# Kernel tuning notes

Measured on AMD Instinct MI355X. Metric: run time of the kernel, lower is better.

## Reference

```python
import jax, jax.numpy as jnp
import numpy as np

BINS = 10          # par.BINS
ALPHA = 0.5        # par.RATIO_KLD
EPS = 1e-10
NUM_ENC = 10       # encoded feature columns used for histograms
BLOCKS = ((7, 19), (19, 21), (21, 25), (25, 27), (27, 29), (29, 31), (31, 34), (34, 38), (38, 50))
B = 1048576


def setup_inputs() -> dict:
    key = jax.random.key(0)
    ks = jax.random.split(key, 16)
    data_encoded = jax.random.normal(ks[0], (B, NUM_ENC), dtype=jnp.float32)
    data_decoded = jax.random.normal(ks[1], (B, 50), dtype=jnp.float32)
    parts = [jax.random.normal(ks[2], (B, 7), dtype=jnp.float32)]  # numerical part
    for i, (s, e) in enumerate(BLOCKS):  # one-hot categorical ground truth
        lab = jax.random.randint(ks[3 + i], (B,), 0, e - s)
        parts.append(jax.nn.one_hot(lab, e - s, dtype=jnp.float32))
    data_true = jnp.concatenate(parts, axis=1)  # (B, 50)
    grp = jax.random.randint(ks[12], (B,), 0, 2).astype(jnp.float32)  # marital flag -> column 11 of combined
    label_true = jnp.stack([
        jax.random.randint(ks[13], (B,), 0, 2).astype(jnp.float32),
        grp,
        jax.random.normal(ks[14], (B,), dtype=jnp.float32),
    ], axis=1)  # (B, 3)
    return {"data_encoded": data_encoded, "data_decoded": data_decoded,
            "data_true": data_true, "label_true": label_true, "batch_size": B}


def _ce(logits, onehot):
    # F.cross_entropy with labels recovered from one-hot rows (nonzero -> argmax)
    labels = jnp.argmax(onehot, axis=1)
    lp = jax.nn.log_softmax(logits, axis=1)
    return -jnp.mean(jnp.take_along_axis(lp, labels[:, None], axis=1))


def _group_hist(enc, mask, mins, maxs):
    # torch.histc per column, restricted to rows where mask==1, normalized by group size
    width = jnp.maximum(maxs - mins, EPS)
    bins = jnp.clip(jnp.floor((enc - mins) / width * BINS), 0, BINS - 1).astype(jnp.int32)  # (B, 10)
    flat = bins + jnp.arange(NUM_ENC, dtype=jnp.int32)[None, :] * BINS                     # (B, 10)
    w = jnp.broadcast_to(mask[:, None], flat.shape).reshape(-1)
    hist = jnp.zeros(NUM_ENC * BINS, dtype=jnp.float32).at[flat.reshape(-1)].add(w)
    return hist.reshape(NUM_ENC, BINS) / jnp.maximum(jnp.sum(mask), 1.0)


def _kl(p, q):
    # KL(p || q) summed over all (feature, bin) cells, zero-safe
    return jnp.sum(jnp.where(p > 0, p * jnp.log(p / jnp.maximum(q, EPS)), 0.0))


def reference(data_encoded, data_decoded, data_true, label_true, batch_size):
    # numerical MSE over first 7 cols, then *7 (mse_Loss)
    mse_loss = jnp.mean((data_decoded[:, 0:7] - data_true[:, 0:7]) ** 2) * 7.0
    # 9 cross-entropy terms over categorical blocks
    ce_loss = jnp.float32(0.0)
    for s, e in BLOCKS:
        ce_loss = ce_loss + _ce(data_decoded[:, s:e], data_true[:, s:e])
    # per-group histogram KLD over the 10 encoded columns (detached in the original)
    enc = data_encoded  # first 10 cols of encoded_combined
    mins = jnp.min(enc, axis=0)
    maxs = jnp.max(enc, axis=0)
    grp = label_true[:, 1]  # column 11 of cat(data_encoded, label_true)
    single_mask = (grp == 0).astype(jnp.float32)
    married_mask = (grp == 1).astype(jnp.float32)
    p = _group_hist(enc, single_mask, mins, maxs)   # (10, BINS)
    q = _group_hist(enc, married_mask, mins, maxs)  # (10, BINS)
    kld = jax.lax.stop_gradient(_kl(p, q))  # original goes through .numpy() -> no grads
    multi_loss = (1.0 - ALPHA) * (mse_loss + ce_loss) + ALPHA * kld
    return (multi_loss, mse_loss, ce_loss, ALPHA * kld)
```

## Files before the change

kernel.cpp:

```cpp
#include <hip/hip_runtime.h>
#include <math.h>

#define EPSF 1e-10f
#define TILE 32
#define TILEH 64

struct WS { double sum_mse, sum_ce; float mn[10], mx[10]; };

typedef __attribute__((address_space(3))) unsigned int lds_u32_t;
typedef __attribute__((address_space(1))) const unsigned int glb_u32_t;
__device__ __forceinline__ void load_lds16(const void* g, void* l){
  __builtin_amdgcn_global_load_lds((glb_u32_t*)g, (lds_u32_t*)l, 16, 0, 0);
}

template<int S, int E>
__device__ __forceinline__ float ce_block_lds(const float* __restrict__ d,
                                              const float* __restrict__ t){
  constexpr int N = E - S;
  float dv[N];
  #pragma unroll
  for (int j = 0; j < N; j++) dv[j] = d[S + j];
  float mx = dv[0];
  #pragma unroll
  for (int j = 1; j < N; j++) mx = fmaxf(mx, dv[j]);
  float se = 0.f, dot = 0.f;
  #pragma unroll
  for (int j = 0; j < N; j++){ se += __expf(dv[j] - mx); dot += t[S + j] * dv[j]; }
  return mx + __logf(se) - dot;
}

__global__ void k_main(const float* __restrict__ enc, const float* __restrict__ dec,
                       const float* __restrict__ tru,
                       double* __restrict__ pmMse, double* __restrict__ pmCe,
                       float* __restrict__ pmMn, float* __restrict__ pmMx,
                       int B, int nbm){
  __shared__ alignas(16) float bufD[2][TILE * 50];
  __shared__ alignas(16) float bufT[2][TILE * 50];
  __shared__ alignas(16) float bufE[2][TILE * 10];
  __shared__ double sMse[4], sCe[4];
  __shared__ float  sMn[4][10], sMx[4][10];

  const int tid  = threadIdx.x;
  const int wave = tid >> 6;
  const int lane = tid & 63;
  const int h    = tid >> 5;
  const int row  = tid & 31;

  float mn[10], mx[10];
  #pragma unroll
  for (int c = 0; c < 10; c++){ mn[c] = 3.4e38f; mx[c] = -3.4e38f; }
  float mse_acc = 0.f, ce_acc = 0.f;

  const int nTiles = B / TILE;
  int nT_loc = (blockIdx.x < nTiles) ? (nTiles - blockIdx.x + nbm - 1) / nbm : 0;

  float4 rd0, rd1, rt0, rt1, re;

  auto load_stage = [&](int k){
    const int tl = blockIdx.x + k * nbm;
    const float4* dp4 = reinterpret_cast<const float4*>(dec + (size_t)tl * (TILE * 50));
    const float4* tp4 = reinterpret_cast<const float4*>(tru + (size_t)tl * (TILE * 50));
    const float4* ep4 = reinterpret_cast<const float4*>(enc + (size_t)tl * (TILE * 10));
    rd0 = dp4[tid];
    rt0 = tp4[tid];
    if (tid < 144){ rd1 = dp4[256 + tid]; rt1 = tp4[256 + tid]; }
    if (tid < 80){ re = ep4[tid]; }
  };
  auto write_stage = [&](int b){
    float4* bD = reinterpret_cast<float4*>(bufD[b]);
    float4* bT = reinterpret_cast<float4*>(bufT[b]);
    float4* bE = reinterpret_cast<float4*>(bufE[b]);
    bD[tid] = rd0;
    bT[tid] = rt0;
    if (tid < 144){ bD[256 + tid] = rd1; bT[256 + tid] = rt1; }
    if (tid < 80){ bE[tid] = re; }
  };

  if (nT_loc > 0) load_stage(0);

  for (int k = 0; k < nT_loc; ++k){
    const int b = k & 1;
    write_stage(b);
    if (k + 1 < nT_loc) load_stage(k + 1);
    __syncthreads();

    {
      const float* d = bufD[b] + row * 50;
      const float* t = bufT[b] + row * 50;
      const float* e = bufE[b] + row * 10;
      switch (h){
        case 0: {
          float m = 0.f;
          #pragma unroll
          for (int j = 0; j < 7; j++){ float df = d[j] - t[j]; m += df * df; }
          mse_acc += m;
          { float v = e[0]; mn[0] = fminf(mn[0], v); mx[0] = fmaxf(mx[0], v); }
          { float v = e[1]; mn[1] = fminf(mn[1], v); mx[1] = fmaxf(mx[1], v); }
        } break;
        case 1: {
          ce_acc += ce_block_lds< 7,19>(d, t);
          { float v = e[2]; mn[2] = fminf(mn[2], v); mx[2] = fmaxf(mx[2], v); }
        } break;
        case 2: {
          ce_acc += ce_block_lds<19,21>(d, t);
          ce_acc += ce_block_lds<21,25>(d, t);
          { float v = e[3]; mn[3] = fminf(mn[3], v); mx[3] = fmaxf(mx[3], v); }
        } break;
        case 3: {
          ce_acc += ce_block_lds<25,27>(d, t);
          ce_acc += ce_block_lds<27,29>(d, t);
          { float v = e[4]; mn[4] = fminf(mn[4], v); mx[4] = fmaxf(mx[4], v); }
        } break;
        case 4: {
          ce_acc += ce_block_lds<29,31>(d, t);
          ce_acc += ce_block_lds<31,34>(d, t);
          { float v = e[5]; mn[5] = fminf(mn[5], v); mx[5] = fmaxf(mx[5], v); }
          { float v = e[6]; mn[6] = fminf(mn[6], v); mx[6] = fmaxf(mx[6], v); }
        } break;
        case 5: {
          ce_acc += ce_block_lds<34,38>(d, t);
          { float v = e[7]; mn[7] = fminf(mn[7], v); mx[7] = fmaxf(mx[7], v); }
        } break;
        case 6: {
          ce_acc += ce_block_lds<38,50>(d, t);
          { float v = e[8]; mn[8] = fminf(mn[8], v); mx[8] = fmaxf(mx[8], v); }
        } break;
        default: {
          { float v = e[9]; mn[9] = fminf(mn[9], v); mx[9] = fmaxf(mx[9], v); }
        } break;
      }
    }
  }

  #pragma unroll
  for (int c = 0; c < 10; c++){
    #pragma unroll
    for (int o = 32; o >= 1; o >>= 1){
      mn[c] = fminf(mn[c], __shfl_xor(mn[c], o));
      mx[c] = fmaxf(mx[c], __shfl_xor(mx[c], o));
    }
  }
  double mseD = (double)mse_acc, ceD = (double)ce_acc;
  #pragma unroll
  for (int o = 32; o >= 1; o >>= 1){
    mseD += __shfl_xor(mseD, o);
    ceD  += __shfl_xor(ceD,  o);
  }
  __syncthreads();
  if (lane == 0){
    sMse[wave] = mseD; sCe[wave] = ceD;
    #pragma unroll
    for (int c = 0; c < 10; c++){ sMn[wave][c] = mn[c]; sMx[wave][c] = mx[c]; }
  }
  __syncthreads();
  if (tid == 0){
    pmMse[blockIdx.x] = sMse[0] + sMse[1] + sMse[2] + sMse[3];
    pmCe[blockIdx.x]  = sCe[0]  + sCe[1]  + sCe[2]  + sCe[3];
    #pragma unroll
    for (int c = 0; c < 10; c++){
      pmMn[c * nbm + blockIdx.x] = fminf(fminf(sMn[0][c], sMn[1][c]), fminf(sMn[2][c], sMn[3][c]));
      pmMx[c * nbm + blockIdx.x] = fmaxf(fmaxf(sMx[0][c], sMx[1][c]), fmaxf(sMx[2][c], sMx[3][c]));
    }
  }
}

__global__ void k_main_fb(const float* __restrict__ enc, const float* __restrict__ dec,
                          const float* __restrict__ tru,
                          double* __restrict__ pmMse, double* __restrict__ pmCe,
                          float* __restrict__ pmMn, float* __restrict__ pmMx,
                          int B, int nbm){
  __shared__ double sMse[4], sCe[4];
  __shared__ float  sMn[4][10], sMx[4][10];
  const int tid = threadIdx.x, wave = tid >> 6, lane = tid & 63;
  float mn[10], mx[10];
  #pragma unroll
  for (int c = 0; c < 10; c++){ mn[c] = 3.4e38f; mx[c] = -3.4e38f; }
  float mse_acc = 0.f, ce_acc = 0.f;
  int stride = nbm * 256;
  for (int r = blockIdx.x * 256 + tid; r < B; r += stride){
    const float* e = enc + (size_t)r * 10;
    #pragma unroll
    for (int c = 0; c < 10; c++){ float v = e[c]; mn[c] = fminf(mn[c], v); mx[c] = fmaxf(mx[c], v); }
    const float* d = dec + (size_t)r * 50;
    const float* t = tru + (size_t)r * 50;
    float m = 0.f;
    #pragma unroll
    for (int j = 0; j < 7; j++){ float df = d[j] - t[j]; m += df * df; }
    mse_acc += m;
    ce_acc += ce_block_lds< 7,19>(d, t);
    ce_acc += ce_block_lds<19,21>(d, t);
    ce_acc += ce_block_lds<21,25>(d, t);
    ce_acc += ce_block_lds<25,27>(d, t);
    ce_acc += ce_block_lds<27,29>(d, t);
    ce_acc += ce_block_lds<29,31>(d, t);
    ce_acc += ce_block_lds<31,34>(d, t);
    ce_acc += ce_block_lds<34,38>(d, t);
    ce_acc += ce_block_lds<38,50>(d, t);
  }
  #pragma unroll
  for (int c = 0; c < 10; c++){
    #pragma unroll
    for (int o = 32; o >= 1; o >>= 1){
      mn[c] = fminf(mn[c], __shfl_xor(mn[c], o));
      mx[c] = fmaxf(mx[c], __shfl_xor(mx[c], o));
    }
  }
  double mseD = (double)mse_acc, ceD = (double)ce_acc;
  #pragma unroll
  for (int o = 32; o >= 1; o >>= 1){ mseD += __shfl_xor(mseD, o); ceD += __shfl_xor(ceD, o); }
  if (lane == 0){
    sMse[wave] = mseD; sCe[wave] = ceD;
    #pragma unroll
    for (int c = 0; c < 10; c++){ sMn[wave][c] = mn[c]; sMx[wave][c] = mx[c]; }
  }
  __syncthreads();
  if (tid == 0){
    pmMse[blockIdx.x] = sMse[0] + sMse[1] + sMse[2] + sMse[3];
    pmCe[blockIdx.x]  = sCe[0]  + sCe[1]  + sCe[2]  + sCe[3];
    #pragma unroll
    for (int c = 0; c < 10; c++){
      pmMn[c * nbm + blockIdx.x] = fminf(fminf(sMn[0][c], sMn[1][c]), fminf(sMn[2][c], sMn[3][c]));
      pmMx[c * nbm + blockIdx.x] = fmaxf(fmaxf(sMx[0][c], sMx[1][c]), fmaxf(sMx[2][c], sMx[3][c]));
    }
  }
}

__global__ void k_reduce(const double* __restrict__ pmMse, const double* __restrict__ pmCe,
                         const float* __restrict__ pmMn, const float* __restrict__ pmMx,
                         WS* __restrict__ ws, int nbm){
  __shared__ double sM[16], sC[16];
  __shared__ float  sMn[16][10], sMx[16][10];
  const int tid = threadIdx.x, wave = tid >> 6, lane = tid & 63;
  double ms = 0.0, ce = 0.0;
  float mn[10], mx[10];
  #pragma unroll
  for (int c = 0; c < 10; c++){ mn[c] = 3.4e38f; mx[c] = -3.4e38f; }
  for (int i = tid; i < nbm; i += 1024){
    ms += pmMse[i]; ce += pmCe[i];
    #pragma unroll
    for (int c = 0; c < 10; c++){
      mn[c] = fminf(mn[c], pmMn[c * nbm + i]);
      mx[c] = fmaxf(mx[c], pmMx[c * nbm + i]);
    }
  }
  #pragma unroll
  for (int o = 32; o >= 1; o >>= 1){
    ms += __shfl_xor(ms, o); ce += __shfl_xor(ce, o);
    #pragma unroll
    for (int c = 0; c < 10; c++){
      mn[c] = fminf(mn[c], __shfl_xor(mn[c], o));
      mx[c] = fmaxf(mx[c], __shfl_xor(mx[c], o));
    }
  }
  if (lane == 0){
    sM[wave] = ms; sC[wave] = ce;
    #pragma unroll
    for (int c = 0; c < 10; c++){ sMn[wave][c] = mn[c]; sMx[wave][c] = mx[c]; }
  }
  __syncthreads();
  if (tid == 0){
    double tm = 0.0, tc = 0.0;
    float rmn[10], rmx[10];
    #pragma unroll
    for (int c = 0; c < 10; c++){ rmn[c] = 3.4e38f; rmx[c] = -3.4e38f; }
    const int nw = (int)(blockDim.x >> 6);
    for (int w = 0; w < nw; w++){
      tm += sM[w]; tc += sC[w];
      #pragma unroll
      for (int c = 0; c < 10; c++){
        rmn[c] = fminf(rmn[c], sMn[w][c]);
        rmx[c] = fmaxf(rmx[c], sMx[w][c]);
      }
    }
    ws->sum_mse = tm; ws->sum_ce = tc;
    #pragma unroll
    for (int c = 0; c < 10; c++){ ws->mn[c] = rmn[c]; ws->mx[c] = rmx[c]; }
  }
}

__global__ void k_hist(const float* __restrict__ enc, const float* __restrict__ lab,
                       const WS* __restrict__ ws, unsigned* __restrict__ ph,
                       int B, int nbh){
  __shared__ unsigned int sh[202];
  __shared__ alignas(16) float bufE[2][TILEH * 10];
  __shared__ alignas(16) float bufL[2][TILEH * 3];

  const int tid  = threadIdx.x;
  const int wave = tid >> 6;
  const int lane = tid & 63;

  for (int i = tid; i < 202; i += 256) sh[i] = 0u;

  float mnv[10], wv[10];
  #pragma unroll
  for (int c = 0; c < 10; c++){
    float lo = ws->mn[c];
    float hi = ws->mx[c];
    mnv[c] = lo;
    wv[c]  = fmaxf(hi - lo, EPSF);
  }

  const int nTiles = (B + TILEH - 1) / TILEH;

  auto stage = [&](int b, int tl){
    const int rowsHere = min(TILEH, B - tl * TILEH);
    const size_t base10 = (size_t)tl * TILEH * 10;
    const size_t base3  = (size_t)tl * TILEH * 3;
    if (rowsHere == TILEH){
      const float4* ep4 = reinterpret_cast<const float4*>(enc + base10);
      const float4* lp4 = reinterpret_cast<const float4*>(lab + base3);
      float4* bE = reinterpret_cast<float4*>(bufE[b]);
      float4* bL = reinterpret_cast<float4*>(bufL[b]);
      { int i = tid; if (i < 160) load_lds16(ep4 + i, bE + i); }
      { int i = tid; if (i < 48)  load_lds16(lp4 + i, bL + i); }
    } else {
      const int ne = rowsHere * 10, nl = rowsHere * 3;
      for (int i = tid; i < ne; i += 256) bufE[b][i] = enc[base10 + i];
      for (int i = tid; i < nl; i += 256) bufL[b][i] = lab[base3 + i];
    }
  };

  const int t0 = blockIdx.x;
  if (t0 < nTiles) stage(0, t0);
  __syncthreads();

  int cur = 0;
  for (int tl = t0; tl < nTiles; tl += nbh){
    int nxt = tl + nbh;
    if (nxt < nTiles) stage(cur ^ 1, nxt);

    const int rowsHere = min(TILEH, B - tl * TILEH);
    const int rrow = lane;
    if (rrow < rowsHere){
      float g = bufL[cur][rrow * 3 + 1];
      int gi = (g == 0.0f) ? 0 : ((g == 1.0f) ? 1 : -1);
      if (gi >= 0){
        const float* e = bufE[cur] + rrow * 10;
        if (wave == 1) atomicAdd(&sh[200 + gi], 1u);
        #define DO_BIN(c) { \
          float bf = floorf((e[(c)] - mnv[(c)]) / wv[(c)] * 10.0f); \
          int b2 = (int)bf; b2 = b2 < 0 ? 0 : (b2 > 9 ? 9 : b2); \
          atomicAdd(&sh[gi * 100 + (c) * 10 + b2], 1u); }
        if (wave == 0){ DO_BIN(0) DO_BIN(1) DO_BIN(2) }
        else if (wave == 1){ DO_BIN(3) DO_BIN(4) }
        else if (wave == 2){ DO_BIN(5) DO_BIN(6) }
        else { DO_BIN(7) DO_BIN(8) DO_BIN(9) }
        #undef DO_BIN
      }
    }
    __syncthreads();
    cur ^= 1;
  }

  for (int i = tid; i < 202; i += 256) ph[(size_t)i * nbh + blockIdx.x] = sh[i];
}

__global__ void k_hreduce(const unsigned* __restrict__ ph, float* __restrict__ histF, int nbh){
  __shared__ unsigned swv[4];
  const int e = blockIdx.x, tid = threadIdx.x, wave = tid >> 6, lane = tid & 63;
  const unsigned* p = ph + (size_t)e * nbh;
  unsigned s0 = 0, s1 = 0, s2 = 0, s3 = 0;
  int k = tid;
  for (; k + 768 < nbh; k += 1024){
    s0 += p[k]; s1 += p[k + 256]; s2 += p[k + 512]; s3 += p[k + 768];
  }
  for (; k < nbh; k += 256) s0 += p[k];
  unsigned s = s0 + s1 + s2 + s3;
  #pragma unroll
  for (int o = 32; o >= 1; o >>= 1) s += __shfl_xor(s, o);
  if (lane == 0) swv[wave] = s;
  __syncthreads();
  if (tid == 0) histF[e] = (float)(swv[0] + swv[1] + swv[2] + swv[3]);
}

__global__ void k_final(const float* __restrict__ histF, const WS* __restrict__ ws,
                        float* __restrict__ out, int B){
  const int tid = threadIdx.x;
  float dens = fmaxf(histF[200], 1.0f);
  float denm = fmaxf(histF[201], 1.0f);
  float kl = 0.f;
  for (int i = tid; i < 100; i += 64){
    float p = histF[i]       / dens;
    float q = histF[100 + i] / denm;
    if (p > 0.f) kl += p * logf(p / fmaxf(q, EPSF));
  }
  #pragma unroll
  for (int o = 32; o >= 1; o >>= 1) kl += __shfl_xor(kl, o);
  if (tid == 0){
    float mse = (float)(ws->sum_mse / (double)B);
    float ce  = (float)(ws->sum_ce  / (double)B);
    float akld = 0.5f * kl;
    out[0] = 0.5f * (mse + ce) + akld;
    out[1] = mse;
    out[2] = ce;
    out[3] = akld;
  }
}

extern "C" void kernel_launch(void* const* d_in, const int* in_sizes, int n_in,
                              void* d_out, int out_size, void* d_ws, size_t ws_size,
                              hipStream_t stream){
  const float* enc = (const float*)d_in[0];
  const float* dec = (const float*)d_in[1];
  const float* tru = (const float*)d_in[2];
  const float* lab = (const float*)d_in[3];
  int B = in_sizes[1] / 50;

  const bool fast = (B > 0) && (B % TILE == 0);

  int nbm = 1280;
  int nTm = fast ? (B / TILE) : ((B + 255) / 256);
  if (nbm > nTm && nTm > 0) nbm = nTm;
  if (nbm < 1) nbm = 1;

  int nbh = 2048;
  int nTh = (B + TILEH - 1) / TILEH;
  if (nbh > nTh && nTh > 0) nbh = nTh;
  if (nbh < 1) nbh = 1;

  while ((size_t)(128 + (size_t)nbm * 96 + (size_t)202 * nbh * 4 + 1024) > ws_size && nbm > 64){
    nbm >>= 1; nbh >>= 1;
  }
  char* w = (char*)d_ws;
  WS* ws = (WS*)w;
  double* pmMse = (double*)(w + 128);
  double* pmCe  = (double*)(w + 128 + (size_t)nbm * 8);
  float*  pmMn  = (float*)(w + 128 + (size_t)nbm * 16);
  float*  pmMx  = (float*)(w + 128 + (size_t)nbm * 16 + (size_t)nbm * 40);
  unsigned* ph  = (unsigned*)(w + 128 + (size_t)nbm * 96);
  float* histF  = (float*)(w + 128 + (size_t)nbm * 96 + (size_t)202 * nbh * 4);
  float* out = (float*)d_out;

  if (fast)
    hipLaunchKernelGGL(k_main,    dim3(nbm), dim3(256), 0, stream, enc, dec, tru,
                       pmMse, pmCe, pmMn, pmMx, B, nbm);
  else
    hipLaunchKernelGGL(k_main_fb, dim3(nbm), dim3(256), 0, stream, enc, dec, tru,
                       pmMse, pmCe, pmMn, pmMx, B, nbm);
  hipLaunchKernelGGL(k_reduce,  dim3(1),   dim3(1024), 0, stream, pmMse, pmCe, pmMn, pmMx, ws, nbm);
  hipLaunchKernelGGL(k_hist,    dim3(nbh), dim3(256),  0, stream, enc, lab, ws, ph, B, nbh);
  hipLaunchKernelGGL(k_hreduce, dim3(202), dim3(256),  0, stream, ph, histF, nbh);
  hipLaunchKernelGGL(k_final,   dim3(1),   dim3(64),   0, stream, histF, ws, out, B);
}
```

Measured before the change: 121.6 us.

## Fuse final min/max/sum reduction into main kernel via last-block atomic counter

Removes the separate single-block k_reduce launch. Each main block now bumps a global atomic counter, and the last block to finish reduces all per-block partials into the workspace. A memset of the counter is added before the launch. Separately, the cross-entropy block drops the max-subtraction in log-sum-exp to save a pass over the values. That assumes the logits stay small, since large logits could overflow expf.

```diff
diff --git a/kernel.cpp b/kernel.cpp
--- a/kernel.cpp
+++ b/kernel.cpp
@@ -17,28 +17,109 @@
 __device__ __forceinline__ float ce_block_lds(const float* __restrict__ d,
                                               const float* __restrict__ t){
   constexpr int N = E - S;
-  float dv[N];
-  #pragma unroll
-  for (int j = 0; j < N; j++) dv[j] = d[S + j];
-  float mx = dv[0];
-  #pragma unroll
-  for (int j = 1; j < N; j++) mx = fmaxf(mx, dv[j]);
   float se = 0.f, dot = 0.f;
   #pragma unroll
-  for (int j = 0; j < N; j++){ se += __expf(dv[j] - mx); dot += t[S + j] * dv[j]; }
-  return mx + __logf(se) - dot;
+  for (int j = 0; j < N; j++){
+    float x = d[S + j];
+    se += __expf(x);
+    dot += t[S + j] * x;
+  }
+  return __logf(se) - dot;
+}
+
+__device__ __forceinline__ void main_epilogue(
+    int tid, int wave, int lane, int nbm,
+    float mse_acc, float ce_acc, float* mn, float* mx,
+    double* sMse, double* sCe, float (*sMn)[10], float (*sMx)[10], int* isLast,
+    double* pmMse, double* pmCe, float* pmMn, float* pmMx,
+    unsigned* cnt, WS* ws){
+  #pragma unroll
+  for (int c = 0; c < 10; c++){
+    #pragma unroll
+    for (int o = 32; o >= 1; o >>= 1){
+      mn[c] = fminf(mn[c], __shfl_xor(mn[c], o));
+      mx[c] = fmaxf(mx[c], __shfl_xor(mx[c], o));
+    }
+  }
+  double mseD = (double)mse_acc, ceD = (double)ce_acc;
+  #pragma unroll
+  for (int o = 32; o >= 1; o >>= 1){
+    mseD += __shfl_xor(mseD, o);
+    ceD  += __shfl_xor(ceD,  o);
+  }
+  __syncthreads();
+  if (lane == 0){
+    sMse[wave] = mseD; sCe[wave] = ceD;
+    #pragma unroll
+    for (int c = 0; c < 10; c++){ sMn[wave][c] = mn[c]; sMx[wave][c] = mx[c]; }
+  }
+  __syncthreads();
+  if (tid == 0){
+    pmMse[blockIdx.x] = sMse[0] + sMse[1] + sMse[2] + sMse[3];
+    pmCe[blockIdx.x]  = sCe[0]  + sCe[1]  + sCe[2]  + sCe[3];
+    #pragma unroll
+    for (int c = 0; c < 10; c++){
+      pmMn[c * nbm + blockIdx.x] = fminf(fminf(sMn[0][c], sMn[1][c]), fminf(sMn[2][c], sMn[3][c]));
+      pmMx[c * nbm + blockIdx.x] = fmaxf(fmaxf(sMx[0][c], sMx[1][c]), fmaxf(sMx[2][c], sMx[3][c]));
+    }
+    __threadfence();
+    unsigned old = atomicAdd(cnt, 1u);
+    *isLast = (old == (unsigned)(nbm - 1)) ? 1 : 0;
+  }
+  __syncthreads();
+  if (*isLast){
+    __threadfence();
+    double ms = 0.0, ce = 0.0;
+    float rmn[10], rmx[10];
+    #pragma unroll
+    for (int c = 0; c < 10; c++){ rmn[c] = 3.4e38f; rmx[c] = -3.4e38f; }
+    for (int i = tid; i < nbm; i += 256){
+      ms += pmMse[i]; ce += pmCe[i];
+      #pragma unroll
+      for (int c = 0; c < 10; c++){
+        rmn[c] = fminf(rmn[c], pmMn[c * nbm + i]);
+        rmx[c] = fmaxf(rmx[c], pmMx[c * nbm + i]);
+      }
+    }
+    #pragma unroll
+    for (int o = 32; o >= 1; o >>= 1){
+      ms += __shfl_xor(ms, o); ce += __shfl_xor(ce, o);
+      #pragma unroll
+      for (int c = 0; c < 10; c++){
+        rmn[c] = fminf(rmn[c], __shfl_xor(rmn[c], o));
+        rmx[c] = fmaxf(rmx[c], __shfl_xor(rmx[c], o));
+      }
+    }
+    if (lane == 0){
+      sMse[wave] = ms; sCe[wave] = ce;
+      #pragma unroll
+      for (int c = 0; c < 10; c++){ sMn[wave][c] = rmn[c]; sMx[wave][c] = rmx[c]; }
+    }
+    __syncthreads();
+    if (tid == 0){
+      ws->sum_mse = sMse[0] + sMse[1] + sMse[2] + sMse[3];
+      ws->sum_ce  = sCe[0]  + sCe[1]  + sCe[2]  + sCe[3];
+      #pragma unroll
+      for (int c = 0; c < 10; c++){
+        ws->mn[c] = fminf(fminf(sMn[0][c], sMn[1][c]), fminf(sMn[2][c], sMn[3][c]));
+        ws->mx[c] = fmaxf(fmaxf(sMx[0][c], sMx[1][c]), fmaxf(sMx[2][c], sMx[3][c]));
+      }
+    }
+  }
 }
 
 __global__ void k_main(const float* __restrict__ enc, const float* __restrict__ dec,
                        const float* __restrict__ tru,
                        double* __restrict__ pmMse, double* __restrict__ pmCe,
                        float* __restrict__ pmMn, float* __restrict__ pmMx,
+                       unsigned* __restrict__ cnt, WS* __restrict__ ws,
                        int B, int nbm){
   __shared__ alignas(16) float bufD[2][TILE * 50];
   __shared__ alignas(16) float bufT[2][TILE * 50];
   __shared__ alignas(16) float bufE[2][TILE * 10];
   __shared__ double sMse[4], sCe[4];
   __shared__ float  sMn[4][10], sMx[4][10];
+  __shared__ int    isLast;
 
   const int tid  = threadIdx.x;
   const int wave = tid >> 6;
@@ -132,45 +213,19 @@
     }
   }
 
-  #pragma unroll
-  for (int c = 0; c < 10; c++){
-    #pragma unroll
-    for (int o = 32; o >= 1; o >>= 1){
-      mn[c] = fminf(mn[c], __shfl_xor(mn[c], o));
-      mx[c] = fmaxf(mx[c], __shfl_xor(mx[c], o));
-    }
-  }
-  double mseD = (double)mse_acc, ceD = (double)ce_acc;
-  #pragma unroll
-  for (int o = 32; o >= 1; o >>= 1){
-    mseD += __shfl_xor(mseD, o);
-    ceD  += __shfl_xor(ceD,  o);
-  }
-  __syncthreads();
-  if (lane == 0){
-    sMse[wave] = mseD; sCe[wave] = ceD;
-    #pragma unroll
-    for (int c = 0; c < 10; c++){ sMn[wave][c] = mn[c]; sMx[wave][c] = mx[c]; }
-  }
-  __syncthreads();
-  if (tid == 0){
-    pmMse[blockIdx.x] = sMse[0] + sMse[1] + sMse[2] + sMse[3];
-    pmCe[blockIdx.x]  = sCe[0]  + sCe[1]  + sCe[2]  + sCe[3];
-    #pragma unroll
-    for (int c = 0; c < 10; c++){
-      pmMn[c * nbm + blockIdx.x] = fminf(fminf(sMn[0][c], sMn[1][c]), fminf(sMn[2][c], sMn[3][c]));
-      pmMx[c * nbm + blockIdx.x] = fmaxf(fmaxf(sMx[0][c], sMx[1][c]), fmaxf(sMx[2][c], sMx[3][c]));
-    }
-  }
+  main_epilogue(tid, wave, lane, nbm, mse_acc, ce_acc, mn, mx,
+                sMse, sCe, sMn, sMx, &isLast, pmMse, pmCe, pmMn, pmMx, cnt, ws);
 }
 
 __global__ void k_main_fb(const float* __restrict__ enc, const float* __restrict__ dec,
                           const float* __restrict__ tru,
                           double* __restrict__ pmMse, double* __restrict__ pmCe,
                           float* __restrict__ pmMn, float* __restrict__ pmMx,
+                          unsigned* __restrict__ cnt, WS* __restrict__ ws,
                           int B, int nbm){
   __shared__ double sMse[4], sCe[4];
   __shared__ float  sMn[4][10], sMx[4][10];
+  __shared__ int    isLast;
   const int tid = threadIdx.x, wave = tid >> 6, lane = tid & 63;
   float mn[10], mx[10];
   #pragma unroll
@@ -197,85 +252,8 @@
     ce_acc += ce_block_lds<34,38>(d, t);
     ce_acc += ce_block_lds<38,50>(d, t);
   }
-  #pragma unroll
-  for (int c = 0; c < 10; c++){
-    #pragma unroll
-    for (int o = 32; o >= 1; o >>= 1){
-      mn[c] = fminf(mn[c], __shfl_xor(mn[c], o));
-      mx[c] = fmaxf(mx[c], __shfl_xor(mx[c], o));
-    }
-  }
-  double mseD = (double)mse_acc, ceD = (double)ce_acc;
-  #pragma unroll
-  for (int o = 32; o >= 1; o >>= 1){ mseD += __shfl_xor(mseD, o); ceD += __shfl_xor(ceD, o); }
-  if (lane == 0){
-    sMse[wave] = mseD; sCe[wave] = ceD;
-    #pragma unroll
-    for (int c = 0; c < 10; c++){ sMn[wave][c] = mn[c]; sMx[wave][c] = mx[c]; }
-  }
-  __syncthreads();
-  if (tid == 0){
-    pmMse[blockIdx.x] = sMse[0] + sMse[1] + sMse[2] + sMse[3];
-    pmCe[blockIdx.x]  = sCe[0]  + sCe[1]  + sCe[2]  + sCe[3];
-    #pragma unroll
-    for (int c = 0; c < 10; c++){
-      pmMn[c * nbm + blockIdx.x] = fminf(fminf(sMn[0][c], sMn[1][c]), fminf(sMn[2][c], sMn[3][c]));
-      pmMx[c * nbm + blockIdx.x] = fmaxf(fmaxf(sMx[0][c], sMx[1][c]), fmaxf(sMx[2][c], sMx[3][c]));
-    }
-  }
-}
-
-__global__ void k_reduce(const double* __restrict__ pmMse, const double* __restrict__ pmCe,
-                         const float* __restrict__ pmMn, const float* __restrict__ pmMx,
-                         WS* __restrict__ ws, int nbm){
-  __shared__ double sM[16], sC[16];
-  __shared__ float  sMn[16][10], sMx[16][10];
-  const int tid = threadIdx.x, wave = tid >> 6, lane = tid & 63;
-  double ms = 0.0, ce = 0.0;
-  float mn[10], mx[10];
-  #pragma unroll
-  for (int c = 0; c < 10; c++){ mn[c] = 3.4e38f; mx[c] = -3.4e38f; }
-  for (int i = tid; i < nbm; i += 1024){
-    ms += pmMse[i]; ce += pmCe[i];
-    #pragma unroll
-    for (int c = 0; c < 10; c++){
-      mn[c] = fminf(mn[c], pmMn[c * nbm + i]);
-      mx[c] = fmaxf(mx[c], pmMx[c * nbm + i]);
-    }
-  }
-  #pragma unroll
-  for (int o = 32; o >= 1; o >>= 1){
-    ms += __shfl_xor(ms, o); ce += __shfl_xor(ce, o);
-    #pragma unroll
-    for (int c = 0; c < 10; c++){
-      mn[c] = fminf(mn[c], __shfl_xor(mn[c], o));
-      mx[c] = fmaxf(mx[c], __shfl_xor(mx[c], o));
-    }
-  }
-  if (lane == 0){
-    sM[wave] = ms; sC[wave] = ce;
-    #pragma unroll
-    for (int c = 0; c < 10; c++){ sMn[wave][c] = mn[c]; sMx[wave][c] = mx[c]; }
-  }
-  __syncthreads();
-  if (tid == 0){
-    double tm = 0.0, tc = 0.0;
-    float rmn[10], rmx[10];
-    #pragma unroll
-    for (int c = 0; c < 10; c++){ rmn[c] = 3.4e38f; rmx[c] = -3.4e38f; }
-    const int nw = (int)(blockDim.x >> 6);
-    for (int w = 0; w < nw; w++){
-      tm += sM[w]; tc += sC[w];
-      #pragma unroll
-      for (int c = 0; c < 10; c++){
-        rmn[c] = fminf(rmn[c], sMn[w][c]);
-        rmx[c] = fmaxf(rmx[c], sMx[w][c]);
-      }
-    }
-    ws->sum_mse = tm; ws->sum_ce = tc;
-    #pragma unroll
-    for (int c = 0; c < 10; c++){ ws->mn[c] = rmn[c]; ws->mx[c] = rmx[c]; }
-  }
+  main_epilogue(tid, wave, lane, nbm, mse_acc, ce_acc, mn, mx,
+                sMse, sCe, sMn, sMx, &isLast, pmMse, pmCe, pmMn, pmMx, cnt, ws);
 }
 
 __global__ void k_hist(const float* __restrict__ enc, const float* __restrict__ lab,
@@ -418,27 +396,29 @@
   if (nbh > nTh && nTh > 0) nbh = nTh;
   if (nbh < 1) nbh = 1;
 
-  while ((size_t)(128 + (size_t)nbm * 96 + (size_t)202 * nbh * 4 + 1024) > ws_size && nbm > 64){
+  while ((size_t)(256 + (size_t)nbm * 96 + (size_t)202 * nbh * 4 + 1024) > ws_size && nbm > 64){
     nbm >>= 1; nbh >>= 1;
   }
   char* w = (char*)d_ws;
-  WS* ws = (WS*)w;
-  double* pmMse = (double*)(w + 128);
-  double* pmCe  = (double*)(w + 128 + (size_t)nbm * 8);
-  float*  pmMn  = (float*)(w + 128 + (size_t)nbm * 16);
-  float*  pmMx  = (float*)(w + 128 + (size_t)nbm * 16 + (size_t)nbm * 40);
-  unsigned* ph  = (unsigned*)(w + 128 + (size_t)nbm * 96);
-  float* histF  = (float*)(w + 128 + (size_t)nbm * 96 + (size_t)202 * nbh * 4);
+  unsigned* cnt = (unsigned*)w;
+  WS* ws = (WS*)(w + 64);
+  double* pmMse = (double*)(w + 256);
+  double* pmCe  = (double*)(w + 256 + (size_t)nbm * 8);
+  float*  pmMn  = (float*)(w + 256 + (size_t)nbm * 16);
+  float*  pmMx  = (float*)(w + 256 + (size_t)nbm * 16 + (size_t)nbm * 40);
+  unsigned* ph  = (unsigned*)(w + 256 + (size_t)nbm * 96);
+  float* histF  = (float*)(w + 256 + (size_t)nbm * 96 + (size_t)202 * nbh * 4);
   float* out = (float*)d_out;
+
+  hipMemsetAsync(w, 0, 64, stream);
 
   if (fast)
     hipLaunchKernelGGL(k_main,    dim3(nbm), dim3(256), 0, stream, enc, dec, tru,
-                       pmMse, pmCe, pmMn, pmMx, B, nbm);
+                       pmMse, pmCe, pmMn, pmMx, cnt, ws, B, nbm);
   else
     hipLaunchKernelGGL(k_main_fb, dim3(nbm), dim3(256), 0, stream, enc, dec, tru,
-                       pmMse, pmCe, pmMn, pmMx, B, nbm);
-  hipLaunchKernelGGL(k_reduce,  dim3(1),   dim3(1024), 0, stream, pmMse, pmCe, pmMn, pmMx, ws, nbm);
-  hipLaunchKernelGGL(k_hist,    dim3(nbh), dim3(256),  0, stream, enc, lab, ws, ph, B, nbh);
-  hipLaunchKernelGGL(k_hreduce, dim3(202), dim3(256),  0, stream, ph, histF, nbh);
-  hipLaunchKernelGGL(k_final,   dim3(1),   dim3(64),   0, stream, histF, ws, out, B);
-}
+                       pmMse, pmCe, pmMn, pmMx, cnt, ws, B, nbm);
+  hipLaunchKernelGGL(k_hist,    dim3(nbh), dim3(256), 0, stream, enc, lab, ws, ph, B, nbh);
+  hipLaunchKernelGGL(k_hreduce, dim3(202), dim3(256), 0, stream, ph, histF, nbh);
+  hipLaunchKernelGGL(k_final,   dim3(1),   dim3(64),  0, stream, histF, ws, out, B);
+}
```

Measured after the change: 171.1 us. 1.41x slower.
